# Performance work log

Hardware: AMD Instinct MI355X
Metric: run time of the kernel (lower is better)

## Reference

```python
import jax, jax.numpy as jnp
import numpy as np

GAMMA = 0.5      # temperature from __init__
SOS_ID = 2       # constant <sos> token id
EPS = 1e-10


def setup_inputs() -> dict:
    key = jax.random.key(0)
    ks = jax.random.split(key, 12)
    B, T, E, DY, DZ, V = 64, 32, 100, 200, 500, 32000
    H = DY + DZ
    s = lambda k, shape, sc=1.0: (jax.random.normal(k, shape, jnp.float32) * sc)
    return {
        "z": s(ks[0], (B, DZ), 0.1),
        "labels": jax.random.uniform(ks[1], (B,), jnp.float32),
        "W_fc": s(ks[2], (DY, 1), 0.1),
        "b_fc": s(ks[3], (DY,), 0.1),
        "embed_weight": s(ks[4], (V, E), 0.1),
        "W_ih": s(ks[5], (3 * H, E), 0.05),
        "W_hh": s(ks[6], (3 * H, H), 0.05),
        "b_ih": s(ks[7], (3 * H,), 0.05),
        "b_hh": s(ks[8], (3 * H,), 0.05),
        "W_out": s(ks[9], (V, H), 0.05),
        "b_out": s(ks[10], (V,), 0.05),
        "gumbel_u": jax.random.uniform(ks[11], (T - 1, B, V), jnp.float32),
        "src": jax.random.randint(jax.random.fold_in(key, 99), (T, B), 0, V),
        "src_len": T,
    }


def _gru_step(h, x, W_ih, W_hh, b_ih, b_hh):
    # PyTorch GRU cell: gates ordered (r, z, n)
    gi = x @ W_ih.T + b_ih          # [B, 3H]
    gh = h @ W_hh.T + b_hh          # [B, 3H]
    i_r, i_z, i_n = jnp.split(gi, 3, axis=-1)
    h_r, h_z, h_n = jnp.split(gh, 3, axis=-1)
    r = jax.nn.sigmoid(i_r + h_r)
    zt = jax.nn.sigmoid(i_z + h_z)
    n = jnp.tanh(i_n + r * h_n)
    return (1.0 - zt) * n + zt * h


def reference(z, labels, W_fc, b_fc, embed_weight, W_ih, W_hh, b_ih, b_hh,
              W_out, b_out, gumbel_u, src, src_len):
    B, H = z.shape[0], W_hh.shape[1]
    V = W_out.shape[0]
    # h0 = cat(fc(1 - labels), z)
    h0 = jnp.concatenate([(1.0 - labels)[:, None] @ W_fc.T + b_fc, z], axis=-1)  # [B, H]
    x0 = jnp.broadcast_to(embed_weight[SOS_ID], (B, embed_weight.shape[1]))      # [B, E]

    def step(carry, u):
        h, x = carry
        h = _gru_step(h, x, W_ih, W_hh, b_ih, b_hh)      # [B, H]
        pred = h @ W_out.T + b_out                        # [B, V]
        g = -jnp.log(-jnp.log(u + EPS) + EPS)             # gumbel noise
        y = jax.nn.softmax(pred + g, axis=-1)             # gumbel_softmax, tau=1
        x_next = (y / GAMMA) @ embed_weight               # soft embedding [B, E]
        return (h, x_next), (h, pred)

    (_, _), (outs, preds) = jax.lax.scan(step, (h0, x0), gumbel_u)  # [T-1,B,H], [T-1,B,V]

    dt = z.dtype
    outputs = jnp.concatenate(
        [h0[None], jnp.zeros((1, B, H), dt), outs], axis=0)         # [T+1, B, H]
    predictions = jnp.concatenate(
        [jnp.zeros((1, B, V), dt), preds], axis=0)                  # [T, B, V]
    return outputs, predictions
```

## Files before the change

kernel.cpp:

```cpp
#include <hip/hip_runtime.h>

#define B 64
#define TS 31
#define E 100
#define DY 200
#define DZ 500
#define V 32000
#define H 700
#define HP 704
#define H3 2100
#define XH 800
#define SOS 2
#define OUT_PRED_OFF (33*B*H)
#define NPB 500
#define VCH 125
#define NVCH 256
#define SOFF 15.0f

typedef unsigned short u16;
typedef __attribute__((ext_vector_type(8))) short short8;
typedef __attribute__((ext_vector_type(4))) float f32x4;

__device__ __forceinline__ float sigm(float x) { return 1.f / (1.f + __expf(-x)); }
__device__ __forceinline__ u16 f2b(float f) {
  union { float f; unsigned int u; } c; c.f = f;
  unsigned int u = c.u;
  u16 h = (u16)(u >> 16);
  unsigned int rem = u & 0xFFFFu;
  h += (u16)((rem > 0x8000u) || (rem == 0x8000u && (h & 1)));
  return h;
}

__global__ __launch_bounds__(256) void k_zero(float* __restrict__ out, long n) {
  long i0 = (long)blockIdx.x * 256 + threadIdx.x;
  long st = (long)gridDim.x * 256;
  for (long i = i0; i < n; i += st) out[i] = 0.f;
}

__global__ __launch_bounds__(256) void k0_init(
    const float* __restrict__ z, const float* __restrict__ labels,
    const float* __restrict__ W_fc, const float* __restrict__ b_fc,
    const float* __restrict__ embed, const float* __restrict__ W_ih,
    const float* __restrict__ W_hh, const float* __restrict__ W_out,
    float* __restrict__ out, float* __restrict__ hA, float* __restrict__ WT,
    u16* __restrict__ W2, u16* __restrict__ h_bf,
    float* __restrict__ xacc, float* __restrict__ Zp, float* __restrict__ gh)
{
  long i0 = (long)blockIdx.x * 256 + threadIdx.x;
  long st = (long)gridDim.x * 256;
  for (long i = i0; i < (long)NPB * B; i += st) Zp[i] = 2.f / (float)NPB;
  for (long i = i0; i < (long)B * H3; i += st) gh[i] = 0.f;
  for (long i = i0; i < (long)B * V; i += st) out[OUT_PRED_OFF + i] = 0.f;
  for (long i = i0; i < (long)B * H; i += st) out[B * H + i] = 0.f;
  for (long i = i0; i < (long)B * H; i += st) {
    int b = (int)(i / H), j = (int)(i % H);
    float v = (j < DY) ? (1.f - labels[b]) * W_fc[j] + b_fc[j]
                       : z[b * DZ + (j - DY)];
    hA[i] = v;
    out[i] = v;
  }
  for (long i = i0; i < (long)B * E; i += st) {
    int e = (int)(i % E);
    xacc[i] = embed[SOS * E + e];
  }
  for (long i = i0; i < (long)B * HP; i += st) h_bf[i] = 0;
  for (long i = i0; i < (long)XH * H3; i += st) {
    int k = (int)(i / H3), g = (int)(i % H3);
    WT[i] = (k < E) ? W_ih[(long)g * E + k] : W_hh[(long)g * H + (k - E)];
  }
  for (long i = i0; i < (long)V * HP; i += st) {
    long s8 = i >> 3; int j = (int)(i & 7);
    int lane = (int)(s8 & 63);
    long tmp = s8 >> 6;
    int kk = (int)(tmp % 22);
    long cgrp = tmp / 22;
    int col = (int)(cgrp * 16 + (lane & 15));
    int k = kk * 32 + ((lane >> 4) << 3) + j;
    W2[i] = (k < H) ? f2b(W_out[(size_t)col * H + k]) : (u16)0;
  }
}

__global__ __launch_bounds__(256) void k1a(
    const float* __restrict__ xacc, const float* __restrict__ Zp,
    const float* __restrict__ hin, const float* __restrict__ WT,
    const float* __restrict__ b_ih,
    float* __restrict__ gig, float* __restrict__ gh)
{
  int nt = blockIdx.x, c = blockIdx.y;
  int n = nt * 64 + (threadIdx.x & 63);
  int bq = threadIdx.x >> 6;
  __shared__ float xs[64][100];
  __shared__ float invZ[64];
  if (c == 0) {
    if (threadIdx.x < 64) {
      float s = 0.f;
      for (int u = 0; u < NPB; ++u) s += Zp[(size_t)u * 64 + threadIdx.x];
      invZ[threadIdx.x] = 2.f / s;
    }
    __syncthreads();
  }
  for (int i = threadIdx.x; i < 6400; i += 256) {
    int b = i / 100, kk = i % 100;
    xs[b][kk] = (c == 0) ? xacc[i] * invZ[b] : hin[b * H + (c - 1) * 100 + kk];
  }
  __syncthreads();
  if (n >= H3) return;
  float acc[16];
  #pragma unroll
  for (int bb = 0; bb < 16; ++bb) acc[bb] = 0.f;
  for (int kk = 0; kk < 100; ++kk) {
    float w = WT[(size_t)(c * 100 + kk) * H3 + n];
    #pragma unroll
    for (int bb = 0; bb < 16; ++bb) acc[bb] += xs[bq * 16 + bb][kk] * w;
  }
  if (c == 0) {
    float bi = b_ih[n];
    #pragma unroll
    for (int bb = 0; bb < 16; ++bb) gig[(size_t)(bq * 16 + bb) * H3 + n] = acc[bb] + bi;
  } else {
    #pragma unroll
    for (int bb = 0; bb < 16; ++bb)
      atomicAdd(&gh[(size_t)(bq * 16 + bb) * H3 + n], acc[bb]);
  }
}

__global__ __launch_bounds__(256) void k1br(
    const float* __restrict__ gig, float* __restrict__ gh,
    const float* __restrict__ b_hh, const float* __restrict__ hin,
    float* __restrict__ hout, float* __restrict__ out_h, u16* __restrict__ h_bf,
    float* __restrict__ xacc)
{
  int i = blockIdx.x * 256 + threadIdx.x;
  if (i >= B * H) return;
  if (i < B * E) xacc[i] = 0.f;
  int b = i / H, j = i % H;
  size_t g0 = (size_t)b * H3 + j;
  float ir = gig[g0], iz = gig[g0 + H], in_ = gig[g0 + 2 * H];
  float hr = gh[g0] + b_hh[j];
  float hz = gh[g0 + H] + b_hh[H + j];
  float hn = gh[g0 + 2 * H] + b_hh[2 * H + j];
  gh[g0] = 0.f; gh[g0 + H] = 0.f; gh[g0 + 2 * H] = 0.f;
  float hprev = hin[b * H + j];
  float r  = sigm(ir + hr);
  float zt = sigm(iz + hz);
  float nn = tanhf(in_ + r * hn);
  float hv = (1.f - zt) * nn + zt * hprev;
  hout[b * H + j] = hv;
  out_h[i] = hv;
  h_bf[b * HP + j] = f2b(hv);
}

__global__ __launch_bounds__(256) void k2(
    const u16* __restrict__ h_bf, const u16* __restrict__ W2,
    const float* __restrict__ b_out, const float* __restrict__ gu,
    float* __restrict__ pred, float* __restrict__ w_f, float* __restrict__ Zp)
{
  __shared__ float lzp[64][4];
  const int u = blockIdx.x, tid = threadIdx.x;
  const int wave = tid >> 6, lane = tid & 63, l15 = lane & 15;
  const int col = u * 64 + wave * 16 + l15;
  f32x4 acc[4];
  #pragma unroll
  for (int q = 0; q < 4; ++q) acc[q] = f32x4{0.f, 0.f, 0.f, 0.f};
  const short8* wv2 = (const short8*)W2 + ((size_t)(u * 4 + wave) * 22) * 64 + lane;
  const u16* hp = h_bf + ((lane >> 4) << 3);
  for (int kk = 0; kk < 22; ++kk) {
    short8 bv = wv2[(size_t)kk * 64];
    #pragma unroll
    for (int rt = 0; rt < 4; ++rt) {
      short8 a = *reinterpret_cast<const short8*>(hp + (size_t)(rt * 16 + l15) * HP + kk * 32);
      acc[rt] = __builtin_amdgcn_mfma_f32_16x16x32_bf16(a, bv, acc[rt], 0, 0, 0);
    }
  }
  float bo = b_out[col];
  #pragma unroll
  for (int rt = 0; rt < 4; ++rt) {
    #pragma unroll
    for (int r = 0; r < 4; ++r) {
      int brow = rt * 16 + ((lane >> 4) << 2) + r;
      float pv = acc[rt][r] + bo;
      size_t off = (size_t)brow * V + col;
      __builtin_nontemporal_store(pv, &pred[off]);
      float uu = __builtin_nontemporal_load(&gu[off]);
      float g = -logf(-logf(uu + 1e-10f) + 1e-10f);
      float w = __expf(pv + g - SOFF);
      __builtin_nontemporal_store(w, &w_f[off]);
      float vz = w;
      vz += __shfl_xor(vz, 1); vz += __shfl_xor(vz, 2);
      vz += __shfl_xor(vz, 4); vz += __shfl_xor(vz, 8);
      if (l15 == 0) lzp[brow][wave] = vz;
    }
  }
  __syncthreads();
  if (tid < 64)
    Zp[(size_t)u * 64 + tid] = lzp[tid][0] + lzp[tid][1] + lzp[tid][2] + lzp[tid][3];
}

__global__ __launch_bounds__(256) void k3(
    const float* __restrict__ w_f, const float* __restrict__ embed,
    float* __restrict__ xacc)
{
  int c = blockIdx.x;
  int v0 = c * VCH;
  int e = threadIdx.x & 127, bh = threadIdx.x >> 7;
  __shared__ float ys[64][VCH];
  for (int i = threadIdx.x; i < 64 * VCH; i += 256) {
    int b = i / VCH, vv = i % VCH;
    ys[b][vv] = w_f[(size_t)b * V + v0 + vv];
  }
  __syncthreads();
  if (e >= E) return;
  float acc[32];
  #pragma unroll
  for (int bb = 0; bb < 32; ++bb) acc[bb] = 0.f;
  for (int vv = 0; vv < VCH; ++vv) {
    float w = embed[(size_t)(v0 + vv) * E + e];
    #pragma unroll
    for (int bb = 0; bb < 32; ++bb) acc[bb] += ys[bh * 32 + bb][vv] * w;
  }
  #pragma unroll
  for (int bb = 0; bb < 32; ++bb)
    atomicAdd(&xacc[(size_t)(bh * 32 + bb) * E + e], acc[bb]);
}

extern "C" void kernel_launch(void* const* d_in, const int* in_sizes, int n_in,
                              void* d_out, int out_size, void* d_ws, size_t ws_size,
                              hipStream_t stream) {
  (void)ws_size;
  float* out = (float*)d_out;

  static const long lsz[12] = {32000, 64, 200, 200, 3200000, 210000, 1470000,
                               2100, 2100, 22400000, 32000, 63488000};
  static const int dictP[12]    = {0, 1, 2, 3, 4, 5, 6, 7, 8, 9, 10, 11};
  static const int alpha14P[12] = {13, 10, 0, 4, 8, 2, 1, 6, 5, 3, 7, 9};
  static const int alpha12P[12] = {11, 10, 0, 4, 8, 2, 1, 6, 5, 3, 7, 9};
  auto okperm = [&](const int* p) -> bool {
    for (int i = 0; i < 12; ++i) {
      if (p[i] >= n_in) return false;
      if ((long)in_sizes[p[i]] != lsz[i]) return false;
    }
    return true;
  };
  const int* P_ = nullptr;
  if (okperm(dictP)) P_ = dictP;
  else if (okperm(alpha14P)) P_ = alpha14P;
  else if (okperm(alpha12P)) P_ = alpha12P;
  if (!P_) { k_zero<<<2048, 256, 0, stream>>>(out, (long)out_size); return; }

  const float* z      = (const float*)d_in[P_[0]];
  const float* labels = (const float*)d_in[P_[1]];
  const float* W_fc   = (const float*)d_in[P_[2]];
  const float* b_fc   = (const float*)d_in[P_[3]];
  const float* embed  = (const float*)d_in[P_[4]];
  const float* W_ih   = (const float*)d_in[P_[5]];
  const float* W_hh   = (const float*)d_in[P_[6]];
  const float* b_ih   = (const float*)d_in[P_[7]];
  const float* b_hh   = (const float*)d_in[P_[8]];
  const float* W_out  = (const float*)d_in[P_[9]];
  const float* b_out  = (const float*)d_in[P_[10]];
  const float* gu     = (const float*)d_in[P_[11]];

  char* w = (char*)d_ws;
  auto alloc = [&](size_t bytes) { char* p = w; w += (bytes + 255) & ~(size_t)255; return p; };
  float* hA    = (float*)alloc((size_t)B * H * 4);
  float* hB    = (float*)alloc((size_t)B * H * 4);
  float* WT    = (float*)alloc((size_t)XH * H3 * 4);
  float* gig   = (float*)alloc((size_t)B * H3 * 4);
  float* gh    = (float*)alloc((size_t)B * H3 * 4);
  float* w_f   = (float*)alloc((size_t)B * V * 4);
  float* Zp    = (float*)alloc((size_t)NPB * B * 4);
  float* xacc  = (float*)alloc((size_t)B * E * 4);
  u16*  W2     = (u16*)alloc((size_t)V * HP * 2);
  u16*  h_bf   = (u16*)alloc((size_t)B * HP * 2);

  k0_init<<<2048, 256, 0, stream>>>(z, labels, W_fc, b_fc, embed, W_ih, W_hh, W_out,
                                    out, hA, WT, W2, h_bf, xacc, Zp, gh);

  for (int t = 0; t < TS; ++t) {
    float* hin  = (t & 1) ? hB : hA;
    float* hout = (t & 1) ? hA : hB;
    float* pred = out + OUT_PRED_OFF + (size_t)(1 + t) * B * V;
    k1a<<<dim3(33, 8), 256, 0, stream>>>(xacc, Zp, hin, WT, b_ih, gig, gh);
    k1br<<<(B * H + 255) / 256, 256, 0, stream>>>(gig, gh, b_hh, hin, hout,
                                                  out + (size_t)(2 + t) * B * H, h_bf,
                                                  xacc);
    k2<<<NPB, 256, 0, stream>>>(h_bf, W2, b_out, gu + (size_t)t * B * V,
                                pred, w_f, Zp);
    if (t < TS - 1)
      k3<<<NVCH, 256, 0, stream>>>(w_f, embed, xacc);
  }
}
```

Before: 3.964 ms.

## Fuse soft-embedding matmul into logits kernel and split accumulator into four copies

The separate k3 kernel, which read the exp-weights from a global [B,V] buffer and multiplied them by the embedding, is removed. Each k2 block now keeps its 64x64 weight tile in LDS, loads the matching 64 embedding rows, computes partial x contributions and atomically adds them into one of four replicated accumulators, which k1a sums. This drops a global write and read of the weight buffer and one launch per step. In exchange it issues many more atomics (500 blocks each adding 6400 values), partly offset by spreading them across four copies, and adds LDS use to k2.

```diff
diff --git a/kernel.cpp b/kernel.cpp
--- a/kernel.cpp
+++ b/kernel.cpp
@@ -13,8 +13,6 @@
 #define SOS 2
 #define OUT_PRED_OFF (33*B*H)
 #define NPB 500
-#define VCH 125
-#define NVCH 256
 #define SOFF 15.0f
 
 typedef unsigned short u16;
@@ -44,7 +42,7 @@
     const float* __restrict__ W_hh, const float* __restrict__ W_out,
     float* __restrict__ out, float* __restrict__ hA, float* __restrict__ WT,
     u16* __restrict__ W2, u16* __restrict__ h_bf,
-    float* __restrict__ xacc, float* __restrict__ Zp, float* __restrict__ gh)
+    float* __restrict__ xacc4, float* __restrict__ Zp, float* __restrict__ gh)
 {
   long i0 = (long)blockIdx.x * 256 + threadIdx.x;
   long st = (long)gridDim.x * 256;
@@ -59,9 +57,9 @@
     hA[i] = v;
     out[i] = v;
   }
-  for (long i = i0; i < (long)B * E; i += st) {
+  for (long i = i0; i < (long)4 * B * E; i += st) {
     int e = (int)(i % E);
-    xacc[i] = embed[SOS * E + e];
+    xacc4[i] = (i < B * E) ? embed[SOS * E + e] : 0.f;
   }
   for (long i = i0; i < (long)B * HP; i += st) h_bf[i] = 0;
   for (long i = i0; i < (long)XH * H3; i += st) {
@@ -81,7 +79,7 @@
 }
 
 __global__ __launch_bounds__(256) void k1a(
-    const float* __restrict__ xacc, const float* __restrict__ Zp,
+    const float* __restrict__ xacc4, const float* __restrict__ Zp,
     const float* __restrict__ hin, const float* __restrict__ WT,
     const float* __restrict__ b_ih,
     float* __restrict__ gig, float* __restrict__ gh)
@@ -101,7 +99,9 @@
   }
   for (int i = threadIdx.x; i < 6400; i += 256) {
     int b = i / 100, kk = i % 100;
-    xs[b][kk] = (c == 0) ? xacc[i] * invZ[b] : hin[b * H + (c - 1) * 100 + kk];
+    xs[b][kk] = (c == 0)
+        ? (xacc4[i] + xacc4[6400 + i] + xacc4[12800 + i] + xacc4[19200 + i]) * invZ[b]
+        : hin[b * H + (c - 1) * 100 + kk];
   }
   __syncthreads();
   if (n >= H3) return;
@@ -128,11 +128,14 @@
     const float* __restrict__ gig, float* __restrict__ gh,
     const float* __restrict__ b_hh, const float* __restrict__ hin,
     float* __restrict__ hout, float* __restrict__ out_h, u16* __restrict__ h_bf,
-    float* __restrict__ xacc)
+    float* __restrict__ xacc4)
 {
   int i = blockIdx.x * 256 + threadIdx.x;
   if (i >= B * H) return;
-  if (i < B * E) xacc[i] = 0.f;
+  if (i < B * E) {
+    xacc4[i] = 0.f; xacc4[6400 + i] = 0.f;
+    xacc4[12800 + i] = 0.f; xacc4[19200 + i] = 0.f;
+  }
   int b = i / H, j = i % H;
   size_t g0 = (size_t)b * H3 + j;
   float ir = gig[g0], iz = gig[g0 + H], in_ = gig[g0 + 2 * H];
@@ -150,11 +153,15 @@
   h_bf[b * HP + j] = f2b(hv);
 }
 
-__global__ __launch_bounds__(256) void k2(
+__global__ __launch_bounds__(256) void k2cd(
     const u16* __restrict__ h_bf, const u16* __restrict__ W2,
     const float* __restrict__ b_out, const float* __restrict__ gu,
-    float* __restrict__ pred, float* __restrict__ w_f, float* __restrict__ Zp)
-{
+    const float* __restrict__ embed,
+    float* __restrict__ pred, float* __restrict__ Zp,
+    float* __restrict__ xacc4, int do_embed)
+{
+  __shared__ float w_lds[64 * 72];
+  __shared__ float emb_lds[64 * 112];
   __shared__ float lzp[64][4];
   const int u = blockIdx.x, tid = threadIdx.x;
   const int wave = tid >> 6, lane = tid & 63, l15 = lane & 15;
@@ -184,7 +191,7 @@
       float uu = __builtin_nontemporal_load(&gu[off]);
       float g = -logf(-logf(uu + 1e-10f) + 1e-10f);
       float w = __expf(pv + g - SOFF);
-      __builtin_nontemporal_store(w, &w_f[off]);
+      w_lds[brow * 72 + wave * 16 + l15] = w;
       float vz = w;
       vz += __shfl_xor(vz, 1); vz += __shfl_xor(vz, 2);
       vz += __shfl_xor(vz, 4); vz += __shfl_xor(vz, 8);
@@ -194,33 +201,36 @@
   __syncthreads();
   if (tid < 64)
     Zp[(size_t)u * 64 + tid] = lzp[tid][0] + lzp[tid][1] + lzp[tid][2] + lzp[tid][3];
-}
-
-__global__ __launch_bounds__(256) void k3(
-    const float* __restrict__ w_f, const float* __restrict__ embed,
-    float* __restrict__ xacc)
-{
-  int c = blockIdx.x;
-  int v0 = c * VCH;
-  int e = threadIdx.x & 127, bh = threadIdx.x >> 7;
-  __shared__ float ys[64][VCH];
-  for (int i = threadIdx.x; i < 64 * VCH; i += 256) {
-    int b = i / VCH, vv = i % VCH;
-    ys[b][vv] = w_f[(size_t)b * V + v0 + vv];
+  if (!do_embed) return;
+  for (int i = tid; i < 64 * 112; i += 256) {
+    int vv = i / 112, e = i % 112;
+    emb_lds[i] = (e < 100) ? embed[(size_t)(u * 64 + vv) * E + e] : 0.f;
   }
   __syncthreads();
-  if (e >= E) return;
-  float acc[32];
-  #pragma unroll
-  for (int bb = 0; bb < 32; ++bb) acc[bb] = 0.f;
-  for (int vv = 0; vv < VCH; ++vv) {
-    float w = embed[(size_t)(v0 + vv) * E + e];
-    #pragma unroll
-    for (int bb = 0; bb < 32; ++bb) acc[bb] += ys[bh * 32 + bb][vv] * w;
-  }
-  #pragma unroll
-  for (int bb = 0; bb < 32; ++bb)
-    atomicAdd(&xacc[(size_t)(bh * 32 + bb) * E + e], acc[bb]);
+  {
+    const int eg = wave, bb = lane;
+    const int e0 = eg * 28;
+    f32x4 a4[7];
+    #pragma unroll
+    for (int q = 0; q < 7; ++q) a4[q] = f32x4{0.f, 0.f, 0.f, 0.f};
+    for (int vv = 0; vv < 64; ++vv) {
+      float w = w_lds[bb * 72 + vv];
+      #pragma unroll
+      for (int q = 0; q < 7; ++q) {
+        const float* ep = &emb_lds[vv * 112 + e0 + q * 4];
+        a4[q][0] += w * ep[0]; a4[q][1] += w * ep[1];
+        a4[q][2] += w * ep[2]; a4[q][3] += w * ep[3];
+      }
+    }
+    float* xa = xacc4 + (size_t)(u & 3) * 6400 + bb * 100;
+    #pragma unroll
+    for (int q = 0; q < 7; ++q)
+      #pragma unroll
+      for (int ji = 0; ji < 4; ++ji) {
+        int e = e0 + q * 4 + ji;
+        if (e < 100) atomicAdd(&xa[e], a4[q][ji]);
+      }
+  }
 }
 
 extern "C" void kernel_launch(void* const* d_in, const int* in_sizes, int n_in,
@@ -267,26 +277,23 @@
   float* WT    = (float*)alloc((size_t)XH * H3 * 4);
   float* gig   = (float*)alloc((size_t)B * H3 * 4);
   float* gh    = (float*)alloc((size_t)B * H3 * 4);
-  float* w_f   = (float*)alloc((size_t)B * V * 4);
   float* Zp    = (float*)alloc((size_t)NPB * B * 4);
-  float* xacc  = (float*)alloc((size_t)B * E * 4);
+  float* xacc4 = (float*)alloc((size_t)4 * B * E * 4);
   u16*  W2     = (u16*)alloc((size_t)V * HP * 2);
   u16*  h_bf   = (u16*)alloc((size_t)B * HP * 2);
 
   k0_init<<<2048, 256, 0, stream>>>(z, labels, W_fc, b_fc, embed, W_ih, W_hh, W_out,
-                                    out, hA, WT, W2, h_bf, xacc, Zp, gh);
+                                    out, hA, WT, W2, h_bf, xacc4, Zp, gh);
 
   for (int t = 0; t < TS; ++t) {
     float* hin  = (t & 1) ? hB : hA;
     float* hout = (t & 1) ? hA : hB;
     float* pred = out + OUT_PRED_OFF + (size_t)(1 + t) * B * V;
-    k1a<<<dim3(33, 8), 256, 0, stream>>>(xacc, Zp, hin, WT, b_ih, gig, gh);
+    k1a<<<dim3(33, 8), 256, 0, stream>>>(xacc4, Zp, hin, WT, b_ih, gig, gh);
     k1br<<<(B * H + 255) / 256, 256, 0, stream>>>(gig, gh, b_hh, hin, hout,
                                                   out + (size_t)(2 + t) * B * H, h_bf,
-                                                  xacc);
-    k2<<<NPB, 256, 0, stream>>>(h_bf, W2, b_out, gu + (size_t)t * B * V,
-                                pred, w_f, Zp);
-    if (t < TS - 1)
-      k3<<<NVCH, 256, 0, stream>>>(w_f, embed, xacc);
-  }
-}
+                                                  xacc4);
+    k2cd<<<NPB, 256, 0, stream>>>(h_bf, W2, b_out, gu + (size_t)t * B * V,
+                                  embed, pred, Zp, xacc4, (t < TS - 1) ? 1 : 0);
+  }
+}
```

New measurement: 8.551 ms. 116% more time.
